# Kernel optimization log

Hardware: AMD Instinct MI355X
Metric: run time of the kernel (lower is better)

## Reference

```python
import jax, jax.numpy as jnp
import numpy as np

N_NODES = 100000
MAX_DEG = 16
D_IN = 256
D_OUT = 256


def setup_inputs() -> dict:
    key = jax.random.key(0)
    k1, k2, k3, k4, k5 = jax.random.split(key, 5)
    x = jax.random.normal(k1, (N_NODES, D_IN), dtype=jnp.float32)
    # padded edge list: -1 marks padding; first column always valid so degree >= 1
    col0 = jax.random.randint(k2, (N_NODES, 1), 0, N_NODES)
    rest = jax.random.randint(k3, (N_NODES, MAX_DEG - 1), -1, N_NODES)
    edge_index = jnp.concatenate([col0, rest], axis=1).astype(jnp.int64)
    # torch Linear(2*D_IN, D_OUT): weight [D_OUT, 2*D_IN], bias [D_OUT]
    W = jax.random.normal(k4, (D_OUT, 2 * D_IN), dtype=jnp.float32) * 0.05
    b = jax.random.normal(k5, (D_OUT,), dtype=jnp.float32) * 0.05
    return {"x": x, "edge_index": edge_index, "W": W, "b": b}


def reference(x, edge_index, W, b):
    # pad with a zero row so index -1 (padding) gathers zeros, matching torch
    padded = jnp.concatenate([x, jnp.zeros((1, x.shape[1]), dtype=x.dtype)], axis=0)
    neigh = padded[edge_index]  # [N, MAX_DEG, D_IN]
    degree = jnp.sum(edge_index >= 0, axis=-1, keepdims=True).astype(x.dtype)  # [N, 1]
    neigh_agg = jnp.sum(neigh, axis=1) / degree  # mean aggregation, [N, D_IN]
    h = jnp.concatenate([x, neigh_agg], axis=1)  # [N, 2*D_IN]
    return h @ W.T + b
```

## Files before the change

kernel.cpp:

```cpp
#include <hip/hip_runtime.h>
#include <stdint.h>


#define MAX_DEG 16
#define D_IN 256
#define D_OUT 256
#define N_NODES_C 100000
#define BM 64

typedef __attribute__((ext_vector_type(8))) short bf16x8;
typedef __attribute__((ext_vector_type(4))) float f32x4;

typedef const __attribute__((address_space(1))) void* gas_ptr;
typedef __attribute__((address_space(3))) void* las_ptr;

__device__ __forceinline__ uint32_t f2bf(float f) {
    union { float f; uint32_t u; } v; v.f = f;
    uint32_t u = v.u;
    return (u + 0x7FFFu + ((u >> 16) & 1u)) >> 16;
}
__device__ __forceinline__ uint32_t pack2(float lo, float hi) {
    return f2bf(lo) | (f2bf(hi) << 16);
}

__global__ __launch_bounds__(256) void cast_w2f_kernel(
    const float* __restrict__ W, ushort* __restrict__ Wb2f, ushort* __restrict__ y2)
{
    if (blockIdx.x < 64) {
        const int t = blockIdx.x * 256 + threadIdx.x;
        const int cg   = t >> 9;
        const int ks   = (t >> 6) & 7;
        const int lane = t & 63;
        const int quad = lane >> 4, r16 = lane & 15;
        const int c = cg * 16 + r16;
        const int k = ks * 32 + quad * 8;
        const float* src = W + (size_t)(c & 255) * 512 + (c >> 8) * 256 + k;
        float4 v0 = ((const float4*)src)[0];
        float4 v1 = ((const float4*)src)[1];
        uint4 p = { pack2(v0.x, v0.y), pack2(v0.z, v0.w),
                    pack2(v1.x, v1.y), pack2(v1.z, v1.w) };
        *(uint4*)(Wb2f + (size_t)t * 8) = p;
    } else {
        if (threadIdx.x < 32) {
            uint4 z = {0u, 0u, 0u, 0u};
            *(uint4*)(y2 + (size_t)N_NODES_C * 256 + threadIdx.x * 8) = z;
        }
    }
}

#define PINB4(b0, b1, b2, b3) do {                                          \
    const uint4& u0 = *(const uint4*)&(b0);                                 \
    const uint4& u1 = *(const uint4*)&(b1);                                 \
    const uint4& u2 = *(const uint4*)&(b2);                                 \
    const uint4& u3 = *(const uint4*)&(b3);                                 \
    asm volatile("" :: "v"(u0.x), "v"(u0.y), "v"(u0.z), "v"(u0.w),          \
                       "v"(u1.x), "v"(u1.y), "v"(u1.z), "v"(u1.w),          \
                       "v"(u2.x), "v"(u2.y), "v"(u2.z), "v"(u2.w),          \
                       "v"(u3.x), "v"(u3.y), "v"(u3.z), "v"(u3.w));         \
} while (0)

__global__ __launch_bounds__(512, 2) void gemm_xw_kernel(
    const float* __restrict__ x, const ushort* __restrict__ Wb2f,
    const float* __restrict__ bias, ushort* __restrict__ y2,
    float* __restrict__ out)
{
    __shared__ float sX[BM * 256];

    const int tid = threadIdx.x;
    const int node0 = blockIdx.x * BM;
    const int w = tid >> 6;
    const int lane = tid & 63;

    #pragma unroll
    for (int it = 0; it < 8; ++it) {
        const int R = w * 8 + it;
        const int rg = node0 + R;
        const float* rowp = x + (size_t)(rg < N_NODES_C ? rg : N_NODES_C - 1) * D_IN;
        const char* gsrc = (const char*)rowp + ((lane ^ it) << 4);
        __builtin_amdgcn_global_load_lds((gas_ptr)gsrc,
            (las_ptr)((char*)sX + (size_t)R * 1024), 16, 0, 0);
    }

    const int quad = lane >> 4;
    const int r16  = lane & 15;
    const int x7   = r16 & 7;
    const int cb   = (w & 3) * 64;

    float bv[4];
    #pragma unroll
    for (int j = 0; j < 4; ++j)
        bv[j] = bias[cb + j * 16 + r16];

    __syncthreads();

    f32x4 acc[4][4];
    #pragma unroll
    for (int s = 0; s < 4; ++s)
        #pragma unroll
        for (int j = 0; j < 4; ++j)
            acc[s][j] = (f32x4){0.f, 0.f, 0.f, 0.f};

    const char* aB[4];
    #pragma unroll
    for (int s = 0; s < 4; ++s)
        aB[s] = (const char*)sX + (size_t)(s * 16 + r16) * 1024;
    const ushort* bp = Wb2f + ((size_t)(w * 4) * 8 + 0) * 64 * 8 + lane * 8;

    bf16x8 bcur[4], bnxt[4];
    #pragma unroll
    for (int j = 0; j < 4; ++j)
        bcur[j] = *(const bf16x8*)(bp + ((size_t)j * 8 + 0) * 64 * 8);
    PINB4(bcur[0], bcur[1], bcur[2], bcur[3]);

    #pragma unroll
    for (int ks = 0; ks < D_IN / 32; ++ks) {
        if (ks < D_IN / 32 - 1) {
            #pragma unroll
            for (int j = 0; j < 4; ++j)
                bnxt[j] = *(const bf16x8*)(bp + ((size_t)j * 8 + ks + 1) * 64 * 8);
            PINB4(bnxt[0], bnxt[1], bnxt[2], bnxt[3]);
        }
        const int ch = ks * 8 + quad * 2;
        bf16x8 afr[4];
        #pragma unroll
        for (int s = 0; s < 4; ++s) {
            f32x4 lo = *(const f32x4*)(aB[s] + ((ch ^ x7) << 4));
            f32x4 hi = *(const f32x4*)(aB[s] + (((ch + 1) ^ x7) << 4));
            union { uint32_t u[4]; bf16x8 v; } cv;
            cv.u[0] = pack2(lo.x, lo.y);
            cv.u[1] = pack2(lo.z, lo.w);
            cv.u[2] = pack2(hi.x, hi.y);
            cv.u[3] = pack2(hi.z, hi.w);
            afr[s] = cv.v;
        }
        #pragma unroll
        for (int j = 0; j < 4; ++j) {
            acc[0][j] = __builtin_amdgcn_mfma_f32_16x16x32_bf16(afr[0], bcur[j], acc[0][j], 0, 0, 0);
            acc[1][j] = __builtin_amdgcn_mfma_f32_16x16x32_bf16(afr[1], bcur[j], acc[1][j], 0, 0, 0);
            acc[2][j] = __builtin_amdgcn_mfma_f32_16x16x32_bf16(afr[2], bcur[j], acc[2][j], 0, 0, 0);
            acc[3][j] = __builtin_amdgcn_mfma_f32_16x16x32_bf16(afr[3], bcur[j], acc[3][j], 0, 0, 0);
        }
        #pragma unroll
        for (int j = 0; j < 4; ++j) bcur[j] = bnxt[j];
    }

    __syncthreads();
    {
        ushort* sE = (ushort*)sX;
        const int reg_ = (w < 4) ? 0 : 1;
        #pragma unroll
        for (int j = 0; j < 4; ++j) {
            const int c = cb + j * 16 + r16;
            #pragma unroll
            for (int s = 0; s < 4; ++s)
                #pragma unroll
                for (int r = 0; r < 4; ++r) {
                    const int row = s * 16 + quad * 4 + r;
                    const float v = acc[s][j][r] + (reg_ ? 0.f : bv[j]);
                    const int a = reg_ * 16384 + row * 256 +
                                  ((((c >> 3) ^ (row & 7)) << 3) | (c & 7));
                    sE[a] = (ushort)f2bf(v);
                }
        }
    }
    __syncthreads();
    {
        const ushort* sE = (const ushort*)sX;
        #pragma unroll
        for (int t = 0; t < 8; ++t) {
            const int idx = t * 512 + tid;
            const int reg_ = idx >> 11;
            const int rowch = idx & 2047;
            const int row = rowch >> 5;
            const int ch  = rowch & 31;
            const int rg = node0 + row;
            if (rg < N_NODES_C) {
                const uint4 v = *(const uint4*)(sE + reg_ * 16384 + row * 256 +
                                                ((ch ^ (row & 7)) << 3));
                char* dst = reg_ == 0
                    ? (char*)(out + (size_t)rg * D_OUT) + ch * 16
                    : (char*)y2 + (size_t)rg * 512 + ch * 16;
                *(uint4*)dst = v;
            }
        }
    }
}

__global__ __launch_bounds__(256, 5) void gather_add_kernel(
    const ushort* __restrict__ y2, const int* __restrict__ edge,
    float* __restrict__ out)
{
    __shared__ char sBuf[4 * 8 * 1024];

    const int w4   = threadIdx.x >> 6;
    const int lane = threadIdx.x & 63;
    const int i = blockIdx.x * 4 + w4;

    const int e = edge[(size_t)i * MAX_DEG + (lane & 15)];
    const unsigned long long vm = __ballot(e >= 0);
    const int deg = (int)__popcll(vm & 0xFFFFull);
    const float inv = 1.0f / (float)deg;

    const uint32_t off_me = (uint32_t)(e < 0 ? N_NODES_C : e) * 512u;
    const char* yb = (const char*)y2;
    const uint32_t coff = (uint32_t)((lane & 31) * 16);
    const int half = lane >> 5;

    const int cw = (lane & 31) * 8 + half * 4;
    float* op = out + (size_t)i * D_OUT + cw;
    const uint2 y1p = *(const uint2*)((const char*)(out + (size_t)i * D_OUT) + cw * 2);

    char* lw = sBuf + (size_t)w4 * 8192;
    #pragma unroll
    for (int k = 0; k < 8; ++k) {
        const uint32_t ro = (uint32_t)__shfl((int)off_me, 2 * k + half, 64);
        const char* gsrc = yb + (size_t)(ro + coff);
        __builtin_amdgcn_global_load_lds((gas_ptr)gsrc, (las_ptr)(lw + k * 1024),
                                         16, 0, 0);
    }
    asm volatile("s_waitcnt vmcnt(0)" ::: "memory");
    __builtin_amdgcn_sched_barrier(0);

    float a[8];
    #pragma unroll
    for (int q = 0; q < 8; ++q) a[q] = 0.f;
    #pragma unroll
    for (int k = 0; k < 8; ++k) {
        uint4 g = *(const uint4*)(lw + k * 1024 + lane * 16);
        uint32_t u[4] = { g.x, g.y, g.z, g.w };
        #pragma unroll
        for (int q = 0; q < 4; ++q) {
            union { uint32_t ui; float f; } lo, hi;
            lo.ui = u[q] << 16;
            hi.ui = u[q] & 0xFFFF0000u;
            a[2*q]   += lo.f;
            a[2*q+1] += hi.f;
        }
    }
    #pragma unroll
    for (int q = 0; q < 8; ++q) a[q] += __shfl_xor(a[q], 32, 64);

    const int q0 = half * 4;
    union { uint32_t ui; float f; } c0, c1, c2, c3;
    c0.ui = y1p.x << 16; c1.ui = y1p.x & 0xFFFF0000u;
    c2.ui = y1p.y << 16; c3.ui = y1p.y & 0xFFFF0000u;
    float4 r;
    r.x = c0.f + inv * a[q0 + 0];
    r.y = c1.f + inv * a[q0 + 1];
    r.z = c2.f + inv * a[q0 + 2];
    r.w = c3.f + inv * a[q0 + 3];
    *(float4*)op = r;
}

#define D_K 512
#define LDS_STRIDE 520

__global__ __launch_bounds__(256) void cast_w_kernel(const float* __restrict__ W,
                                                     ushort* __restrict__ Wb) {
    int i = (blockIdx.x * 256 + threadIdx.x) * 4;
    float4 v = *(const float4*)(W + i);
    ushort4 p = { (ushort)f2bf(v.x), (ushort)f2bf(v.y),
                  (ushort)f2bf(v.z), (ushort)f2bf(v.w) };
    *(ushort4*)(Wb + i) = p;
}

__global__ __launch_bounds__(256) void sage_fp32_kernel(
    const float* __restrict__ x, const int* __restrict__ edge,
    const ushort* __restrict__ Wb, const float* __restrict__ bias,
    float* __restrict__ out)
{
    __shared__ ushort sH[32 * LDS_STRIDE];
    const int tid = threadIdx.x;
    const int node0 = blockIdx.x * 32;
    {
        const int m = tid >> 3, l = tid & 7;
        const int node = node0 + m;
        const float4* xrow = (const float4*)(x + (size_t)node * D_IN);
        ushort* dst = sH + m * LDS_STRIDE + l * 32;
        #pragma unroll
        for (int q = 0; q < 8; ++q) {
            float4 v = xrow[l * 8 + q];
            ushort4 p = { (ushort)f2bf(v.x), (ushort)f2bf(v.y),
                          (ushort)f2bf(v.z), (ushort)f2bf(v.w) };
            *(ushort4*)(dst + q * 4) = p;
        }
        float4 agg[8];
        #pragma unroll
        for (int q = 0; q < 8; ++q) agg[q] = make_float4(0.f,0.f,0.f,0.f);
        int deg = 0;
        for (int d = 0; d < MAX_DEG; ++d) {
            int nb = edge[(size_t)node * MAX_DEG + d];
            if (nb >= 0) {
                ++deg;
                const float4* nr = (const float4*)(x + (size_t)nb * D_IN);
                #pragma unroll
                for (int q = 0; q < 8; ++q) {
                    float4 t = nr[l * 8 + q];
                    agg[q].x += t.x; agg[q].y += t.y;
                    agg[q].z += t.z; agg[q].w += t.w;
                }
            }
        }
        const float inv = 1.0f / (float)deg;
        ushort* dst2 = sH + m * LDS_STRIDE + D_IN + l * 32;
        #pragma unroll
        for (int q = 0; q < 8; ++q) {
            ushort4 p = { (ushort)f2bf(agg[q].x*inv), (ushort)f2bf(agg[q].y*inv),
                          (ushort)f2bf(agg[q].z*inv), (ushort)f2bf(agg[q].w*inv) };
            *(ushort4*)(dst2 + q * 4) = p;
        }
    }
    __syncthreads();
    {
        const int wave = tid >> 6, lane = tid & 63;
        const int quad = lane >> 4, r16 = lane & 15;
        const int mt = wave & 1, nh = wave >> 1;
        f32x4 acc[8];
        #pragma unroll
        for (int j = 0; j < 8; ++j) {
            float bv = bias[(nh * 8 + j) * 16 + r16];
            acc[j] = (f32x4){bv, bv, bv, bv};
        }
        const ushort* arow = sH + (mt * 16 + r16) * LDS_STRIDE + quad * 8;
        #pragma unroll
        for (int ks = 0; ks < D_K / 32; ++ks) {
            bf16x8 a = *(const bf16x8*)(arow + ks * 32);
            #pragma unroll
            for (int j = 0; j < 8; ++j) {
                const int o = (nh * 8 + j) * 16 + r16;
                bf16x8 b = *(const bf16x8*)(Wb + (size_t)o * D_K + ks * 32 + quad * 8);
                acc[j] = __builtin_amdgcn_mfma_f32_16x16x32_bf16(a, b, acc[j], 0, 0, 0);
            }
        }
        #pragma unroll
        for (int j = 0; j < 8; ++j) {
            const int o = (nh * 8 + j) * 16 + r16;
            #pragma unroll
            for (int r = 0; r < 4; ++r) {
                const int row = node0 + mt * 16 + quad * 4 + r;
                out[(size_t)row * D_OUT + o] = acc[j][r];
            }
        }
    }
}

extern "C" void kernel_launch(void* const* d_in, const int* in_sizes, int n_in,
                              void* d_out, int out_size, void* d_ws, size_t ws_size,
                              hipStream_t stream) {
    const float* x    = (const float*)d_in[0];
    const int*   edge = (const int*)d_in[1];
    const float* W    = (const float*)d_in[2];
    const float* bias = (const float*)d_in[3];
    float* out = (float*)d_out;

    const size_t y2_bytes = (size_t)(N_NODES_C + 1) * 256 * 2;
    const size_t wb_bytes = (size_t)512 * 256 * 2;
    const int n = in_sizes[0] / D_IN;

    if (ws_size >= y2_bytes + wb_bytes) {
        ushort* y2   = (ushort*)d_ws;
        ushort* Wb2f = (ushort*)((char*)d_ws + y2_bytes);
        cast_w2f_kernel<<<65, 256, 0, stream>>>(W, Wb2f, y2);
        gemm_xw_kernel<<<(n + BM - 1) / BM, 512, 0, stream>>>(x, Wb2f, bias, y2, out);
        gather_add_kernel<<<n / 4, 256, 0, stream>>>(y2, edge, out);
    } else {
        ushort* Wb = (ushort*)d_ws;
        cast_w_kernel<<<(D_OUT * D_K) / 1024, 256, 0, stream>>>(W, Wb);
        sage_fp32_kernel<<<n / 32, 256, 0, stream>>>(x, edge, Wb, bias, out);
    }
}
```

Measured before the change: 361.4 us.

## Convert x to bf16 once at load and halve GEMM LDS footprint

```diff
diff --git a/kernel.cpp b/kernel.cpp
--- a/kernel.cpp
+++ b/kernel.cpp
@@ -59,33 +59,52 @@
                        "v"(u3.x), "v"(u3.y), "v"(u3.z), "v"(u3.w));         \
 } while (0)
 
-__global__ __launch_bounds__(512, 2) void gemm_xw_kernel(
+__global__ __launch_bounds__(512, 4) void gemm_xw_kernel(
     const float* __restrict__ x, const ushort* __restrict__ Wb2f,
     const float* __restrict__ bias, ushort* __restrict__ y2,
     float* __restrict__ out)
 {
-    __shared__ float sX[BM * 256];
+    __shared__ ushort sT[BM * 256];
 
     const int tid = threadIdx.x;
     const int node0 = blockIdx.x * BM;
     const int w = tid >> 6;
     const int lane = tid & 63;
-
-    #pragma unroll
-    for (int it = 0; it < 8; ++it) {
-        const int R = w * 8 + it;
-        const int rg = node0 + R;
-        const float* rowp = x + (size_t)(rg < N_NODES_C ? rg : N_NODES_C - 1) * D_IN;
-        const char* gsrc = (const char*)rowp + ((lane ^ it) << 4);
-        __builtin_amdgcn_global_load_lds((gas_ptr)gsrc,
-            (las_ptr)((char*)sX + (size_t)R * 1024), 16, 0, 0);
-    }
-
     const int quad = lane >> 4;
     const int r16  = lane & 15;
     const int x7   = r16 & 7;
     const int cb   = (w & 3) * 64;
 
+    {
+        const int row = tid >> 3, l = tid & 7;
+        const int rg = node0 + row;
+        const float* src = x + (size_t)(rg < N_NODES_C ? rg : N_NODES_C - 1) * D_IN + l * 32;
+        f32x4 v[8];
+        #pragma unroll
+        for (int q = 0; q < 8; ++q) v[q] = ((const f32x4*)src)[q];
+        {
+            const uint4& a0 = *(const uint4*)&v[0]; const uint4& a1 = *(const uint4*)&v[1];
+            const uint4& a2 = *(const uint4*)&v[2]; const uint4& a3 = *(const uint4*)&v[3];
+            const uint4& a4 = *(const uint4*)&v[4]; const uint4& a5 = *(const uint4*)&v[5];
+            const uint4& a6 = *(const uint4*)&v[6]; const uint4& a7 = *(const uint4*)&v[7];
+            asm volatile("" :: "v"(a0.x),"v"(a0.y),"v"(a0.z),"v"(a0.w),
+                               "v"(a1.x),"v"(a1.y),"v"(a1.z),"v"(a1.w),
+                               "v"(a2.x),"v"(a2.y),"v"(a2.z),"v"(a2.w),
+                               "v"(a3.x),"v"(a3.y),"v"(a3.z),"v"(a3.w),
+                               "v"(a4.x),"v"(a4.y),"v"(a4.z),"v"(a4.w),
+                               "v"(a5.x),"v"(a5.y),"v"(a5.z),"v"(a5.w),
+                               "v"(a6.x),"v"(a6.y),"v"(a6.z),"v"(a6.w),
+                               "v"(a7.x),"v"(a7.y),"v"(a7.z),"v"(a7.w));
+        }
+        #pragma unroll
+        for (int q = 0; q < 4; ++q) {
+            uint4 p = { pack2(v[2*q].x, v[2*q].y), pack2(v[2*q].z, v[2*q].w),
+                        pack2(v[2*q+1].x, v[2*q+1].y), pack2(v[2*q+1].z, v[2*q+1].w) };
+            const int c = l * 4 + q;
+            *(uint4*)((char*)sT + row * 512 + ((c ^ (row & 7)) << 4)) = p;
+        }
+    }
+
     float bv[4];
     #pragma unroll
     for (int j = 0; j < 4; ++j)
@@ -100,10 +119,6 @@
         for (int j = 0; j < 4; ++j)
             acc[s][j] = (f32x4){0.f, 0.f, 0.f, 0.f};
 
-    const char* aB[4];
-    #pragma unroll
-    for (int s = 0; s < 4; ++s)
-        aB[s] = (const char*)sX + (size_t)(s * 16 + r16) * 1024;
     const ushort* bp = Wb2f + ((size_t)(w * 4) * 8 + 0) * 64 * 8 + lane * 8;
 
     bf16x8 bcur[4], bnxt[4];
@@ -120,19 +135,11 @@
                 bnxt[j] = *(const bf16x8*)(bp + ((size_t)j * 8 + ks + 1) * 64 * 8);
             PINB4(bnxt[0], bnxt[1], bnxt[2], bnxt[3]);
         }
-        const int ch = ks * 8 + quad * 2;
         bf16x8 afr[4];
         #pragma unroll
-        for (int s = 0; s < 4; ++s) {
-            f32x4 lo = *(const f32x4*)(aB[s] + ((ch ^ x7) << 4));
-            f32x4 hi = *(const f32x4*)(aB[s] + (((ch + 1) ^ x7) << 4));
-            union { uint32_t u[4]; bf16x8 v; } cv;
-            cv.u[0] = pack2(lo.x, lo.y);
-            cv.u[1] = pack2(lo.z, lo.w);
-            cv.u[2] = pack2(hi.x, hi.y);
-            cv.u[3] = pack2(hi.z, hi.w);
-            afr[s] = cv.v;
-        }
+        for (int s = 0; s < 4; ++s)
+            afr[s] = *(const bf16x8*)((const char*)sT + (s * 16 + r16) * 512 +
+                                      (((ks * 4 + quad) ^ x7) << 4));
         #pragma unroll
         for (int j = 0; j < 4; ++j) {
             acc[0][j] = __builtin_amdgcn_mfma_f32_16x16x32_bf16(afr[0], bcur[j], acc[0][j], 0, 0, 0);
@@ -145,9 +152,7 @@
     }
 
     __syncthreads();
-    {
-        ushort* sE = (ushort*)sX;
-        const int reg_ = (w < 4) ? 0 : 1;
+    if (w < 4) {
         #pragma unroll
         for (int j = 0; j < 4; ++j) {
             const int c = cb + j * 16 + r16;
@@ -156,32 +161,46 @@
                 #pragma unroll
                 for (int r = 0; r < 4; ++r) {
                     const int row = s * 16 + quad * 4 + r;
-                    const float v = acc[s][j][r] + (reg_ ? 0.f : bv[j]);
-                    const int a = reg_ * 16384 + row * 256 +
-                                  ((((c >> 3) ^ (row & 7)) << 3) | (c & 7));
-                    sE[a] = (ushort)f2bf(v);
+                    sT[row * 256 + ((((c >> 3) ^ (row & 7)) << 3) | (c & 7))] =
+                        (ushort)f2bf(acc[s][j][r] + bv[j]);
                 }
         }
     }
     __syncthreads();
-    {
-        const ushort* sE = (const ushort*)sX;
-        #pragma unroll
-        for (int t = 0; t < 8; ++t) {
-            const int idx = t * 512 + tid;
-            const int reg_ = idx >> 11;
-            const int rowch = idx & 2047;
-            const int row = rowch >> 5;
-            const int ch  = rowch & 31;
-            const int rg = node0 + row;
-            if (rg < N_NODES_C) {
-                const uint4 v = *(const uint4*)(sE + reg_ * 16384 + row * 256 +
-                                                ((ch ^ (row & 7)) << 3));
-                char* dst = reg_ == 0
-                    ? (char*)(out + (size_t)rg * D_OUT) + ch * 16
-                    : (char*)y2 + (size_t)rg * 512 + ch * 16;
-                *(uint4*)dst = v;
-            }
+    #pragma unroll
+    for (int t = 0; t < 4; ++t) {
+        const int idx = t * 512 + tid;
+        const int row = idx >> 5, ch = idx & 31;
+        const int rg = node0 + row;
+        if (rg < N_NODES_C) {
+            const uint4 v = *(const uint4*)(sT + row * 256 + ((ch ^ (row & 7)) << 3));
+            *(uint4*)((char*)(out + (size_t)rg * D_OUT) + ch * 16) = v;
+        }
+    }
+    __syncthreads();
+    if (w >= 4) {
+        #pragma unroll
+        for (int j = 0; j < 4; ++j) {
+            const int c = cb + j * 16 + r16;
+            #pragma unroll
+            for (int s = 0; s < 4; ++s)
+                #pragma unroll
+                for (int r = 0; r < 4; ++r) {
+                    const int row = s * 16 + quad * 4 + r;
+                    sT[row * 256 + ((((c >> 3) ^ (row & 7)) << 3) | (c & 7))] =
+                        (ushort)f2bf(acc[s][j][r]);
+                }
+        }
+    }
+    __syncthreads();
+    #pragma unroll
+    for (int t = 0; t < 4; ++t) {
+        const int idx = t * 512 + tid;
+        const int row = idx >> 5, ch = idx & 31;
+        const int rg = node0 + row;
+        if (rg < N_NODES_C) {
+            const uint4 v = *(const uint4*)(sT + row * 256 + ((ch ^ (row & 7)) << 3));
+            *(uint4*)((char*)y2 + (size_t)rg * 512 + ch * 16) = v;
         }
     }
 }
```

Measured after the change: 354.4 us. Within noise of the previous version (-1.9%).
